# Optimization experiments

Hardware: AMD Instinct MI355X
Metric: run time of the kernel (lower is better)

The kernel has to match this reference:

```python
import jax, jax.numpy as jnp
import numpy as np

B, NNODES, NODE, EDGEF, HID, NFACT, DEG = 256, 64, 64, 32, 256, 8, 32
N_TOTAL = B * NNODES            # 16384 nodes
E_TOTAL = B * NNODES * DEG      # 524288 edges
NEDGES_HEAD = 128               # len(self.edges)


def _w(key, shape, fan_in):
    return jax.random.normal(key, shape, dtype=jnp.float32) * (1.0 / np.sqrt(fan_in))


def setup_inputs() -> dict:
    key = jax.random.key(0)
    ks = jax.random.split(key, 16)
    # message-passing edge_index: per graph, node i -> (i+k) % NNODES, k=1..DEG
    src = np.repeat(np.arange(NNODES), DEG)
    dst = (src + np.tile(np.arange(1, DEG + 1), NNODES)) % NNODES
    offs = (np.arange(B) * NNODES)[:, None]
    ei = np.stack([(src[None, :] + offs).reshape(-1),
                   (dst[None, :] + offs).reshape(-1)], axis=0)
    edge_index = jnp.asarray(ei, dtype=jnp.int32)  # [2, E_TOTAL]
    # actor head edge list (within-graph indices): ring distance 1 and 2
    e1 = np.stack([np.arange(NNODES), (np.arange(NNODES) + 1) % NNODES], 1)
    e2 = np.stack([np.arange(NNODES), (np.arange(NNODES) + 2) % NNODES], 1)
    edges = jnp.asarray(np.concatenate([e1, e2], 0), dtype=jnp.int32)  # [128,2]

    D = NODE + HID  # 320
    inp = {
        "x": jax.random.normal(ks[0], (N_TOTAL, NODE), dtype=jnp.float32),
        "edge_index": edge_index,
        "edge_attr": jax.random.normal(ks[1], (E_TOTAL, EDGEF), dtype=jnp.float32),
        "edges": edges,
        "high": jax.random.uniform(ks[2], (NEDGES_HEAD + NFACT,), minval=0.5, maxval=2.0),
        "W1": _w(ks[3], (2 * NODE + EDGEF, HID), 2 * NODE + EDGEF),
        "b1": jnp.zeros((HID,), jnp.float32),
        "W2": _w(ks[4], (HID, HID), HID),
        "b2": jnp.zeros((HID,), jnp.float32),
        "Wmu": _w(ks[5], (2 * D, 1), 2 * D),
        "bmu": jnp.zeros((1,), jnp.float32),
        "Wsig": _w(ks[6], (2 * D, 1), 2 * D),
        "bsig": jnp.zeros((1,), jnp.float32),
        "Wmu2": _w(ks[7], (D, 1), D),
        "bmu2": jnp.zeros((1,), jnp.float32),
        "Wsig2": _w(ks[8], (D, 1), D),
        "bsig2": jnp.zeros((1,), jnp.float32),
    }
    return inp


def reference(x, edge_index, edge_attr, edges, high,
              W1, b1, W2, b2, Wmu, bmu, Wsig, bsig, Wmu2, bmu2, Wsig2, bsig2):
    # EdgeConv (flow='target_to_source', aggr='add'): x_i=x[ei0], x_j=x[ei1], aggregate at ei0
    xi = x[edge_index[0]]                                   # [E, NODE]
    xj = x[edge_index[1]]                                   # [E, NODE]
    msg_in = jnp.concatenate([xi, xj, edge_attr], axis=1)   # [E, 2*NODE+EDGEF]
    msg = jax.nn.relu(msg_in @ W1 + b1) @ W2 + b2           # [E, HID]
    agg = jax.ops.segment_sum(msg, edge_index[0], num_segments=x.shape[0])  # [N, HID]

    x_pp = jnp.concatenate([x, agg], axis=1).reshape(-1, NNODES, NODE + HID)  # [B, nn, D]

    ef_src = x_pp[:, edges[:, 0], :]                        # [B, 128, D]
    ef_dst = x_pp[:, edges[:, 1], :]                        # [B, 128, D]
    ef = jnp.concatenate([ef_src, ef_dst], axis=2)          # [B, 128, 2D]

    alpha = jax.nn.softplus((ef @ Wmu + bmu).squeeze(-1) + 1e-20)    # [B, 128]
    beta = jax.nn.softplus((ef @ Wsig + bsig).squeeze(-1) + 1e-20)   # [B, 128]

    fact = x_pp[:, -NFACT:, :]                              # [B, 8, D]
    alpha2 = jax.nn.softplus((fact @ Wmu2 + bmu2).squeeze(-1) + 1e-20)   # [B, 8]
    beta2 = jax.nn.softplus((fact @ Wsig2 + bsig2).squeeze(-1) + 1e-20)  # [B, 8]

    # deterministic=True path
    alpha = alpha + 1e-20
    beta = beta + 1e-20
    dis_action = alpha / (alpha + beta) * high[:-NFACT]     # [B, 128]
    alpha2 = alpha2 + 1e-20
    beta2 = beta2 + 1e-20
    order_act = alpha2 / (alpha2 + beta2) * high[-NFACT:]   # [B, 8]
    act = jnp.concatenate([dis_action, order_act], axis=-1) # [B, 136]
    return act
```

## Files before the change

### kernel.cpp

```cpp
#include <hip/hip_runtime.h>
#include <math.h>

#define BATCH_  256
#define ETOT    524288

typedef __attribute__((ext_vector_type(8))) short short8v;
typedef __attribute__((ext_vector_type(4))) float f32x4;

#define MFMA16(a,b,c) __builtin_amdgcn_mfma_f32_16x16x32_bf16((a),(b),(c),0,0,0)

__device__ __forceinline__ unsigned short f2bf(float f) {
    unsigned int x = __float_as_uint(f);
    return (unsigned short)((x + 0x7fffu + ((x >> 16) & 1u)) >> 16);
}
__device__ __forceinline__ float bf2f(unsigned short h) {
    return __uint_as_float(((unsigned int)h) << 16);
}
__device__ __forceinline__ float softplus_f(float v) {
    return v > 20.f ? v : log1pf(expf(v));
}
__device__ __forceinline__ float dot4(f32x4 a, f32x4 b) {
    float z = a[0] * b[0];
    z = fmaf(a[1], b[1], z);
    z = fmaf(a[2], b[2], z);
    z = fmaf(a[3], b[3], z);
    return z;
}
__device__ __forceinline__ void packfrag(f32x4 a, f32x4 q, short8v& hi, short8v& lo) {
    float v[8] = {a[0], a[1], a[2], a[3], q[0], q[1], q[2], q[3]};
#pragma unroll
    for (int j = 0; j < 8; j++) {
        const unsigned short h = f2bf(v[j]);
        hi[j] = (short)h;
        lo[j] = (short)f2bf(v[j] - bf2f(h));
    }
}

__global__ __launch_bounds__(256) void k_prep(const float* __restrict__ W1,
                                              const float* __restrict__ W2,
                                              unsigned short* __restrict__ frags) {
    const int u = blockIdx.x;
    const float* S = (u < 80) ? W1 : W2;
    const int ul = (u < 80) ? u : (u - 80);
    const int rowbase = (ul >> 4) * 32;
    const int cht = ul & 15;
    for (int idx = threadIdx.x; idx < 512; idx += 256) {
        const int l = idx >> 3, j = idx & 7;
        const int row = rowbase + ((l >> 4) << 3) + j;
        const int col = cht * 16 + (l & 15);
        const float v = S[row * 256 + col];
        const unsigned short h = f2bf(v);
        frags[u * 1024 + idx]       = h;
        frags[u * 1024 + 512 + idx] = f2bf(v - bf2f(h));
    }
}

__global__ __launch_bounds__(512) __attribute__((amdgpu_waves_per_eu(2)))
void k_fused(
    const float* __restrict__ x, const float* __restrict__ ea,
    const int* __restrict__ dst, const int* __restrict__ edges,
    const float* __restrict__ high, const float* __restrict__ b1,
    const float* __restrict__ b2, const unsigned short* __restrict__ frags,
    const float* __restrict__ Wmu,  const float* __restrict__ bmu,
    const float* __restrict__ Wsig, const float* __restrict__ bsig,
    const float* __restrict__ Wmu2, const float* __restrict__ bmu2,
    const float* __restrict__ Wsig2,const float* __restrict__ bsig2,
    float* __restrict__ out)
{
    __shared__ __align__(16) unsigned char smem[131072];
    float*          s_xwb   = (float*)smem;
    unsigned short* s_ea    = (unsigned short*)(smem + 65536);
    unsigned char*  s_dstl  = (unsigned char*)(smem + 98304);
    float*          s_sumh1 = (float*)smem;
    float*          s_agg   = (float*)(smem + 65536);
    float*          s_su    = (float*)smem;
    float*          s_su2   = (float*)(smem + 1024);

    const int b = blockIdx.x, tid = threadIdx.x;
    const int l = tid & 63, w = tid >> 6, g = l >> 4, l15 = l & 15;
    const int ng = w & 3, cq = w >> 2;
    const int node = ng * 16 + l15;
    const int swzn = (l15 & 7) << 2;

    for (int idx = tid; idx < 2048; idx += 512)
        s_dstl[idx] = (unsigned char)(dst[b * 2048 + idx] & 63);

    const int ols = tid >> 8;
    const int ns  = (tid & 255) >> 2;
    const int ko  = tid & 3;
    const int sll = (ko << 4) | (ns & 15), sng = ns >> 4;
    const float* eab = ea + (size_t)b * 65536 + (size_t)ns * 1024 + ko * 8;

    f32x4 ld0 = *(const f32x4*)&eab[(size_t)ols * 32];
    f32x4 ld1 = *(const f32x4*)&eab[(size_t)ols * 32 + 4];

    short8v Xh[2], Xl[2];
#pragma unroll
    for (int kt = 0; kt < 2; kt++) {
        const float* p = x + (size_t)(b * 64 + node) * 64 + kt * 32 + g * 8;
        packfrag(*(const f32x4*)p, *(const f32x4*)(p + 4), Xh[kt], Xl[kt]);
    }

    f32x4 xab1[8];
#pragma unroll
    for (int i = 0; i < 8; i++) {
        const int cht = cq * 8 + i;
        f32x4 d = *(const f32x4*)&b1[cht * 16 + g * 4];
#pragma unroll
        for (int kt = 0; kt < 2; kt++) {
            const int base = (kt * 16 + cht) * 1024 + l * 8;
            const short8v Ahh = *(const short8v*)&frags[base];
            const short8v All = *(const short8v*)&frags[base + 512];
            d = MFMA16(All, Xh[kt], d);
            d = MFMA16(Ahh, Xl[kt], d);
            d = MFMA16(Ahh, Xh[kt], d);
        }
        xab1[i] = d;
    }

#pragma unroll
    for (int i = 0; i < 8; i++) {
        const int cht = cq * 8 + i;
        f32x4 d = {0.f, 0.f, 0.f, 0.f};
#pragma unroll
        for (int kt = 0; kt < 2; kt++) {
            const int base = ((kt + 2) * 16 + cht) * 1024 + l * 8;
            const short8v Ahh = *(const short8v*)&frags[base];
            const short8v All = *(const short8v*)&frags[base + 512];
            d = MFMA16(All, Xh[kt], d);
            d = MFMA16(Ahh, Xl[kt], d);
            d = MFMA16(Ahh, Xh[kt], d);
        }
        *(f32x4*)&s_xwb[node * 256 + ((cht * 16 + g * 4) ^ swzn)] = d;
    }

    short8v Ah[8], Al[8];
#pragma unroll
    for (int i = 0; i < 8; i++) {
        const int base = (64 + cq * 8 + i) * 1024 + l * 8;
        Ah[i] = *(const short8v*)&frags[base];
        Al[i] = *(const short8v*)&frags[base + 512];
    }

    {
        short8v hi, lo;
        packfrag(ld0, ld1, hi, lo);
        *(short8v*)&s_ea[((((0 * 2 + 0) * 2 + ols) * 4 + sng) * 64 + sll) * 8] = hi;
        *(short8v*)&s_ea[((((0 * 2 + 1) * 2 + ols) * 4 + sng) * 64 + sll) * 8] = lo;
    }
    ld0 = *(const f32x4*)&eab[(size_t)(2 + ols) * 32];
    ld1 = *(const f32x4*)&eab[(size_t)(2 + ols) * 32 + 4];
    __syncthreads();

    f32x4 acc[8];
#pragma unroll
    for (int i = 0; i < 8; i++) acc[i] = (f32x4){0.f, 0.f, 0.f, 0.f};

    for (int c = 0; c < 16; ++c) {
        if (c < 15) {
            short8v hi, lo;
            packfrag(ld0, ld1, hi, lo);
            const int nb = (c + 1) & 1;
            *(short8v*)&s_ea[((((nb * 2 + 0) * 2 + ols) * 4 + sng) * 64 + sll) * 8] = hi;
            *(short8v*)&s_ea[((((nb * 2 + 1) * 2 + ols) * 4 + sng) * 64 + sll) * 8] = lo;
            if (c < 14) {
                const int o = (c + 2) * 2 + ols;
                ld0 = *(const f32x4*)&eab[(size_t)o * 32];
                ld1 = *(const f32x4*)&eab[(size_t)o * 32 + 4];
            }
        }

        const int cb2 = c & 1;
        const unsigned short dw = ((const unsigned short*)s_dstl)[node * 16 + c];

#pragma unroll
        for (int ol = 0; ol < 2; ol++) {
            const short8v Bh = *(const short8v*)&s_ea[((((cb2 * 2 + 0) * 2 + ol) * 4 + ng) * 64 + l) * 8];
            const short8v Bl = *(const short8v*)&s_ea[((((cb2 * 2 + 1) * 2 + ol) * 4 + ng) * 64 + l) * 8];
            const int d = (dw >> (ol * 8)) & 0xFF;
            const int swz = (d & 7) << 2;

#pragma unroll
            for (int i = 0; i < 8; i++) {
                const int cb = cq * 128 + i * 16 + g * 4;
                const f32x4 wb = *(const f32x4*)&s_xwb[d * 256 + (cb ^ swz)];
                f32x4 di = MFMA16(Al[i], Bh, xab1[i]);
                di = MFMA16(Ah[i], Bl, di);
                di = MFMA16(Ah[i], Bh, di);
#pragma unroll
                for (int r = 0; r < 4; r++)
                    acc[i][r] += fmaxf(di[r] + wb[r], 0.f);
            }
        }
        __syncthreads();
    }

#pragma unroll
    for (int i = 0; i < 8; i++)
        *(f32x4*)&s_sumh1[node * 256 + ((cq * 128 + i * 16 + g * 4) ^ swzn)] = acc[i];
    __syncthreads();

    const int rt = w & 3, ch8 = w >> 2;
    f32x4 acc2[8];
#pragma unroll
    for (int j = 0; j < 8; j++) acc2[j] = (f32x4){0.f, 0.f, 0.f, 0.f};

    for (int ks = 0; ks < 8; ks++) {
        const int row = rt * 16 + l15;
        const int cbk = ks * 32 + g * 8;
        const f32x4 a0 = *(const f32x4*)&s_sumh1[row * 256 + (cbk ^ swzn)];
        const f32x4 a1 = *(const f32x4*)&s_sumh1[row * 256 + ((cbk + 4) ^ swzn)];
        short8v Ahh, All;
        packfrag(a0, a1, Ahh, All);
#pragma unroll
        for (int j = 0; j < 8; j++) {
            const int base = (80 + ks * 16 + ch8 * 8 + j) * 1024 + l * 8;
            const short8v Bh = *(const short8v*)&frags[base];
            const short8v Bl = *(const short8v*)&frags[base + 512];
            acc2[j] = MFMA16(Ahh, Bh, acc2[j]);
            acc2[j] = MFMA16(Ahh, Bl, acc2[j]);
            acc2[j] = MFMA16(All, Bh, acc2[j]);
        }
    }

#pragma unroll
    for (int j = 0; j < 8; j++) {
        const int col = (ch8 * 8 + j) * 16 + l15;
        const float bb = 32.f * b2[col];
#pragma unroll
        for (int r = 0; r < 4; r++) {
            const int row = rt * 16 + g * 4 + r;
            s_agg[row * 256 + (col ^ ((row & 7) << 2))] = acc2[j][r] + bb;
        }
    }
    __syncthreads();

    if (tid < 256) {
        const int n = tid >> 2, s = tid & 3;
        const float* Wp = ((s & 1) ? Wsig : Wmu) + ((s >> 1) ? 320 : 0);
        const float* xr = x + (size_t)(b * 64 + n) * 64;
        const int sw = (n & 7) << 2;
        float z = 0.f;
#pragma unroll
        for (int kq = 0; kq < 16; kq++)
            z += dot4(*(const f32x4*)&xr[kq * 4], *(const f32x4*)&Wp[kq * 4]);
#pragma unroll 8
        for (int kq = 0; kq < 64; kq++)
            z += dot4(*(const f32x4*)&s_agg[n * 256 + ((kq * 4) ^ sw)],
                      *(const f32x4*)&Wp[64 + kq * 4]);
        s_su[n * 4 + s] = z;
    } else if (tid < 272) {
        const int j = (tid - 256) >> 1, s = tid & 1;
        const int n = 56 + j;
        const float* Wp = s ? Wsig2 : Wmu2;
        const float* xr = x + (size_t)(b * 64 + n) * 64;
        const int sw = (n & 7) << 2;
        float z = 0.f;
#pragma unroll
        for (int kq = 0; kq < 16; kq++)
            z += dot4(*(const f32x4*)&xr[kq * 4], *(const f32x4*)&Wp[kq * 4]);
#pragma unroll 8
        for (int kq = 0; kq < 64; kq++)
            z += dot4(*(const f32x4*)&s_agg[n * 256 + ((kq * 4) ^ sw)],
                      *(const f32x4*)&Wp[64 + kq * 4]);
        s_su2[j * 2 + s] = z;
    }
    __syncthreads();

    if (tid < 128) {
        const int e0 = edges[tid * 2], e1 = edges[tid * 2 + 1];
        const float a  = softplus_f(s_su[e0 * 4 + 0] + s_su[e1 * 4 + 2] + bmu[0])  + 1e-20f;
        const float be = softplus_f(s_su[e0 * 4 + 1] + s_su[e1 * 4 + 3] + bsig[0]) + 1e-20f;
        out[(size_t)b * 136 + tid] = a / (a + be) * high[tid];
    } else if (tid < 136) {
        const int j = tid - 128;
        const float a  = softplus_f(s_su2[j * 2 + 0] + bmu2[0])  + 1e-20f;
        const float be = softplus_f(s_su2[j * 2 + 1] + bsig2[0]) + 1e-20f;
        out[(size_t)b * 136 + tid] = a / (a + be) * high[128 + j];
    }
}

extern "C" void kernel_launch(void* const* d_in, const int* in_sizes, int n_in,
                              void* d_out, int out_size, void* d_ws, size_t ws_size,
                              hipStream_t stream) {
    const float* x     = (const float*)d_in[0];
    const int*   eidx  = (const int*)  d_in[1];
    const float* ea    = (const float*)d_in[2];
    const int*   edges = (const int*)  d_in[3];
    const float* high  = (const float*)d_in[4];
    const float* W1    = (const float*)d_in[5];
    const float* b1    = (const float*)d_in[6];
    const float* W2    = (const float*)d_in[7];
    const float* b2    = (const float*)d_in[8];
    const float* Wmu   = (const float*)d_in[9];
    const float* bmu   = (const float*)d_in[10];
    const float* Wsig  = (const float*)d_in[11];
    const float* bsig  = (const float*)d_in[12];
    const float* Wmu2  = (const float*)d_in[13];
    const float* bmu2  = (const float*)d_in[14];
    const float* Wsig2 = (const float*)d_in[15];
    const float* bsig2 = (const float*)d_in[16];
    float* out = (float*)d_out;

    const size_t frag_off = (ws_size - (size_t)208 * 2048) & ~(size_t)1023;
    unsigned short* frags = (unsigned short*)((char*)d_ws + frag_off);
    const int* dst = eidx + ETOT;

    hipLaunchKernelGGL(k_prep,  dim3(208),    dim3(256), 0, stream, W1, W2, frags);
    hipLaunchKernelGGL(k_fused, dim3(BATCH_), dim3(512), 0, stream,
                       x, ea, dst, edges, high, b1, b2, frags,
                       Wmu, bmu, Wsig, bsig, Wmu2, bmu2, Wsig2, bsig2, out);
}
```

Measured before the change: 73.88 us.

## Split fused kernel into edge-message and head kernels with channel-halved blocks

The single fused per-graph kernel is split in two. The first kernel runs 512 blocks, each handling half of the hidden channels for one graph, with halved LDS and register state and higher waves-per-EU, then writes the per-node hidden sums to global workspace. A second per-graph kernel reloads those sums into swizzled LDS and runs the W2 GEMM and actor heads. This targets low occupancy, since 256 blocks on many CUs leaves compute idle. In exchange it re-reads every edge attribute twice (once per half), adds a global round-trip for the sums, and adds an extra launch.

```diff
diff --git a/kernel.cpp b/kernel.cpp
--- a/kernel.cpp
+++ b/kernel.cpp
@@ -2,6 +2,7 @@
 #include <math.h>
 
 #define BATCH_  256
+#define NTOT    16384
 #define ETOT    524288
 
 typedef __attribute__((ext_vector_type(8))) short short8v;
@@ -55,30 +56,21 @@
     }
 }
 
-__global__ __launch_bounds__(512) __attribute__((amdgpu_waves_per_eu(2)))
-void k_fused(
+__global__ __launch_bounds__(512) __attribute__((amdgpu_waves_per_eu(4)))
+void k_ab(
     const float* __restrict__ x, const float* __restrict__ ea,
-    const int* __restrict__ dst, const int* __restrict__ edges,
-    const float* __restrict__ high, const float* __restrict__ b1,
-    const float* __restrict__ b2, const unsigned short* __restrict__ frags,
-    const float* __restrict__ Wmu,  const float* __restrict__ bmu,
-    const float* __restrict__ Wsig, const float* __restrict__ bsig,
-    const float* __restrict__ Wmu2, const float* __restrict__ bmu2,
-    const float* __restrict__ Wsig2,const float* __restrict__ bsig2,
-    float* __restrict__ out)
+    const int* __restrict__ dst, const float* __restrict__ b1,
+    const unsigned short* __restrict__ frags, float* __restrict__ sumh1)
 {
-    __shared__ __align__(16) unsigned char smem[131072];
-    float*          s_xwb   = (float*)smem;
-    unsigned short* s_ea    = (unsigned short*)(smem + 65536);
-    unsigned char*  s_dstl  = (unsigned char*)(smem + 98304);
-    float*          s_sumh1 = (float*)smem;
-    float*          s_agg   = (float*)(smem + 65536);
-    float*          s_su    = (float*)smem;
-    float*          s_su2   = (float*)(smem + 1024);
-
-    const int b = blockIdx.x, tid = threadIdx.x;
+    __shared__ __align__(16) unsigned char smem[67584];
+    float*          s_xwb  = (float*)smem;
+    unsigned short* s_ea   = (unsigned short*)(smem + 32768);
+    unsigned char*  s_dstl = (unsigned char*)(smem + 65536);
+
+    const int b = blockIdx.x & 255, half = blockIdx.x >> 8;
+    const int tid = threadIdx.x;
     const int l = tid & 63, w = tid >> 6, g = l >> 4, l15 = l & 15;
-    const int ng = w & 3, cq = w >> 2;
+    const int ng = w & 3, cqq = w >> 2;
     const int node = ng * 16 + l15;
     const int swzn = (l15 & 7) << 2;
 
@@ -101,10 +93,10 @@
         packfrag(*(const f32x4*)p, *(const f32x4*)(p + 4), Xh[kt], Xl[kt]);
     }
 
-    f32x4 xab1[8];
-#pragma unroll
-    for (int i = 0; i < 8; i++) {
-        const int cht = cq * 8 + i;
+    f32x4 xab1[4];
+#pragma unroll
+    for (int i = 0; i < 4; i++) {
+        const int cht = half * 8 + cqq * 4 + i;
         f32x4 d = *(const f32x4*)&b1[cht * 16 + g * 4];
 #pragma unroll
         for (int kt = 0; kt < 2; kt++) {
@@ -119,8 +111,8 @@
     }
 
 #pragma unroll
-    for (int i = 0; i < 8; i++) {
-        const int cht = cq * 8 + i;
+    for (int i = 0; i < 4; i++) {
+        const int cht = half * 8 + cqq * 4 + i;
         f32x4 d = {0.f, 0.f, 0.f, 0.f};
 #pragma unroll
         for (int kt = 0; kt < 2; kt++) {
@@ -131,13 +123,13 @@
             d = MFMA16(Ahh, Xl[kt], d);
             d = MFMA16(Ahh, Xh[kt], d);
         }
-        *(f32x4*)&s_xwb[node * 256 + ((cht * 16 + g * 4) ^ swzn)] = d;
-    }
-
-    short8v Ah[8], Al[8];
-#pragma unroll
-    for (int i = 0; i < 8; i++) {
-        const int base = (64 + cq * 8 + i) * 1024 + l * 8;
+        *(f32x4*)&s_xwb[node * 128 + (((cqq * 4 + i) * 16 + g * 4) ^ swzn)] = d;
+    }
+
+    short8v Ah[4], Al[4];
+#pragma unroll
+    for (int i = 0; i < 4; i++) {
+        const int base = (64 + half * 8 + cqq * 4 + i) * 1024 + l * 8;
         Ah[i] = *(const short8v*)&frags[base];
         Al[i] = *(const short8v*)&frags[base + 512];
     }
@@ -152,9 +144,9 @@
     ld1 = *(const f32x4*)&eab[(size_t)(2 + ols) * 32 + 4];
     __syncthreads();
 
-    f32x4 acc[8];
-#pragma unroll
-    for (int i = 0; i < 8; i++) acc[i] = (f32x4){0.f, 0.f, 0.f, 0.f};
+    f32x4 acc[4];
+#pragma unroll
+    for (int i = 0; i < 4; i++) acc[i] = (f32x4){0.f, 0.f, 0.f, 0.f};
 
     for (int c = 0; c < 16; ++c) {
         if (c < 15) {
@@ -181,9 +173,9 @@
             const int swz = (d & 7) << 2;
 
 #pragma unroll
-            for (int i = 0; i < 8; i++) {
-                const int cb = cq * 128 + i * 16 + g * 4;
-                const f32x4 wb = *(const f32x4*)&s_xwb[d * 256 + (cb ^ swz)];
+            for (int i = 0; i < 4; i++) {
+                const int cbl = (cqq * 4 + i) * 16 + g * 4;
+                const f32x4 wb = *(const f32x4*)&s_xwb[d * 128 + (cbl ^ swz)];
                 f32x4 di = MFMA16(Al[i], Bh, xab1[i]);
                 di = MFMA16(Ah[i], Bl, di);
                 di = MFMA16(Ah[i], Bh, di);
@@ -195,9 +187,39 @@
         __syncthreads();
     }
 
-#pragma unroll
-    for (int i = 0; i < 8; i++)
-        *(f32x4*)&s_sumh1[node * 256 + ((cq * 128 + i * 16 + g * 4) ^ swzn)] = acc[i];
+    const size_t grow = (size_t)b * 64 + node;
+#pragma unroll
+    for (int i = 0; i < 4; i++) {
+        const int cg = (half * 8 + cqq * 4 + i) * 16 + g * 4;
+        *(f32x4*)&sumh1[grow * 256 + cg] = acc[i];
+    }
+}
+
+__global__ __launch_bounds__(512) void k_cd(
+    const float* __restrict__ x, const float* __restrict__ sumh1,
+    const int* __restrict__ edges, const float* __restrict__ high,
+    const unsigned short* __restrict__ frags, const float* __restrict__ b2,
+    const float* __restrict__ Wmu,  const float* __restrict__ bmu,
+    const float* __restrict__ Wsig, const float* __restrict__ bsig,
+    const float* __restrict__ Wmu2, const float* __restrict__ bmu2,
+    const float* __restrict__ Wsig2,const float* __restrict__ bsig2,
+    float* __restrict__ out)
+{
+    __shared__ __align__(16) unsigned char smem[131072];
+    float* s_sumh1 = (float*)smem;
+    float* s_agg   = (float*)(smem + 65536);
+    float* s_su    = (float*)smem;
+    float* s_su2   = (float*)(smem + 1024);
+
+    const int b = blockIdx.x, tid = threadIdx.x;
+    const int l = tid & 63, w = tid >> 6, g = l >> 4, l15 = l & 15;
+    const int swzn = (l15 & 7) << 2;
+
+    for (int idx = tid; idx < 4096; idx += 512) {
+        const int row = idx >> 6, c4 = (idx & 63) * 4;
+        const f32x4 v = *(const f32x4*)&sumh1[(size_t)b * 16384 + (size_t)idx * 4];
+        *(f32x4*)&s_sumh1[row * 256 + (c4 ^ ((row & 7) << 2))] = v;
+    }
     __syncthreads();
 
     const int rt = w & 3, ch8 = w >> 2;
@@ -302,12 +324,15 @@
     const float* bsig2 = (const float*)d_in[16];
     float* out = (float*)d_out;
 
+    float* sumh1 = (float*)d_ws;
     const size_t frag_off = (ws_size - (size_t)208 * 2048) & ~(size_t)1023;
     unsigned short* frags = (unsigned short*)((char*)d_ws + frag_off);
     const int* dst = eidx + ETOT;
 
-    hipLaunchKernelGGL(k_prep,  dim3(208),    dim3(256), 0, stream, W1, W2, frags);
-    hipLaunchKernelGGL(k_fused, dim3(BATCH_), dim3(512), 0, stream,
-                       x, ea, dst, edges, high, b1, b2, frags,
+    hipLaunchKernelGGL(k_prep, dim3(208),    dim3(256), 0, stream, W1, W2, frags);
+    hipLaunchKernelGGL(k_ab,   dim3(512),    dim3(512), 0, stream,
+                       x, ea, dst, b1, frags, sumh1);
+    hipLaunchKernelGGL(k_cd,   dim3(BATCH_), dim3(512), 0, stream,
+                       x, sumh1, edges, high, frags, b2,
                        Wmu, bmu, Wsig, bsig, Wmu2, bmu2, Wsig2, bsig2, out);
 }
```

Result: slower. 78.53 us (+6.3%).
